# Performance work log

Measured on AMD Instinct MI355X. Metric: run time of the kernel, lower is better.

Reference implementation:

```python
import jax, jax.numpy as jnp
from jax import lax
import numpy as np

B, S, I, H, O, L = 64, 512, 1024, 1024, 1024, 2


def setup_inputs() -> dict:
    key = jax.random.key(0)
    ks = jax.random.split(key, 12)
    sI = 1.0 / np.sqrt(I)
    sH = 1.0 / np.sqrt(H)
    # weights stored as [in, out] (transpose of torch Linear.weight); same math.
    return {
        "input": jax.random.normal(ks[0], (B, S, I), jnp.float32),
        "Wxz": jax.random.uniform(ks[1], (L, I, H), jnp.float32, -sI, sI),
        "Whz": jax.random.uniform(ks[2], (L, H, H), jnp.float32, -sH, sH),
        "bz": jax.random.uniform(ks[3], (L, H), jnp.float32, -sH, sH),
        "Wxr": jax.random.uniform(ks[4], (L, I, H), jnp.float32, -sI, sI),
        "Whr": jax.random.uniform(ks[5], (L, H, H), jnp.float32, -sH, sH),
        "br": jax.random.uniform(ks[6], (L, H), jnp.float32, -sH, sH),
        "Wxg": jax.random.uniform(ks[7], (L, I, H), jnp.float32, -sI, sI),
        "Whg": jax.random.uniform(ks[8], (L, H, H), jnp.float32, -sH, sH),
        "bg": jax.random.uniform(ks[9], (L, H), jnp.float32, -sH, sH),
        "Why": jax.random.uniform(ks[10], (H, O), jnp.float32, -sH, sH),
        "by": jax.random.uniform(ks[11], (O,), jnp.float32, -sH, sH),
    }


def reference(input, Wxz, Whz, bz, Wxr, Whr, br, Wxg, Whg, bg, Why, by):
    n_layers = Whz.shape[0]
    batch = input.shape[0]
    h_dim = Whz.shape[-1]
    h0 = jnp.zeros((n_layers, batch, h_dim), input.dtype)  # (L,B,H)

    def step(h, xt):  # xt: (B,I)
        new_h = []
        inp = xt
        for l in range(n_layers):  # static, small
            hl = h[l]
            z = jax.nn.sigmoid(inp @ Wxz[l] + hl @ Whz[l] + bz[l])
            r = jax.nn.sigmoid(inp @ Wxr[l] + hl @ Whr[l] + br[l])
            g = jnp.tanh(inp @ Wxg[l] + (r * hl) @ Whg[l] + bg[l])
            hl = z * hl + (1.0 - z) * g
            new_h.append(hl)
            inp = hl
        y = inp @ Why + by  # (B,O)
        return jnp.stack(new_h), y

    hT, ys = lax.scan(step, h0, jnp.swapaxes(input, 0, 1))  # ys: (S,B,O)
    layer_output = jnp.swapaxes(ys, 0, 1)       # (B,S,O)
    hidden_state = jnp.swapaxes(hT, 0, 1)       # (B,L,H)
    return layer_output, hidden_state
```

## Files before the change

### kernel.cpp

```cpp
#include <hip/hip_runtime.h>
#include <cstdint>

using u16 = unsigned short;
using u32 = unsigned int;
using u64 = unsigned long long;

typedef __bf16 bf16x8 __attribute__((ext_vector_type(8)));
typedef float  f32x4  __attribute__((ext_vector_type(4)));
typedef unsigned int u32x4 __attribute__((ext_vector_type(4)));

#define WPITCH 2064
#define SCAN_LDS 124160
#define YG_LDS   147456
#define POLL_BOUND 32768

__device__ __forceinline__ float b2f(u16 u) {
    u32 i = ((u32)u) << 16; float f; __builtin_memcpy(&f, &i, 4); return f;
}
__device__ __forceinline__ u16 f2b(float f) {
    u32 i; __builtin_memcpy(&i, &f, 4);
    u32 r = (i + 0x7FFFu + ((i >> 16) & 1u)) >> 16; return (u16)r;
}
__device__ __forceinline__ uint4 pack8f(const float* f) {
    u16 t[8];
#pragma unroll
    for (int j = 0; j < 8; ++j) t[j] = f2b(f[j]);
    uint4 r; __builtin_memcpy(&r, t, 16); return r;
}

__global__ __launch_bounds__(512) void gru_fused(
    const float* __restrict__ xin,
    const float* __restrict__ Wxz, const float* __restrict__ Wxr,
    const float* __restrict__ Wxg,
    const float* __restrict__ Whz, const float* __restrict__ Whr,
    const float* __restrict__ Whg,
    const float* __restrict__ bzp, const float* __restrict__ brp,
    const float* __restrict__ bgp,
    float* __restrict__ hout,
    float* __restrict__ hidden,
    u16* __restrict__ ring,
    u16* __restrict__ hb,
    u16* __restrict__ rb,
    u32* __restrict__ flags)
{
    extern __shared__ char sm[];
    char*  hs    = sm;
    char*  scZ   = sm + 33024;
    char*  xb0   = sm + 65792;
    char*  xb1   = sm + 82176;
    float* xls   = (float*)(sm + 98560);
    u16*   tmp16 = (u16*)(sm + 123136);

    const int tid   = threadIdx.x;
    const int lane  = tid & 63;
    const int wv    = tid >> 6;
    const int layer = blockIdx.x >> 7;
    const int id    = blockIdx.x & 127;
    const int grp   = id >> 5;
    const int w     = id & 31;
    const int bg0   = grp * 16;
    const int n0w   = w * 32;
    const long wbase = (long)layer * 1048576;
    const long bbase = (long)layer * 1024;

    u16* hbG = hb + (layer * 4 + grp) * 16384;
    u16* rbG = rb + (layer * 4 + grp) * 16384;
    u32* f_rh   = flags + ((layer * 4 + grp) * 2 + 0) * 512;
    u32* f_h    = flags + ((layer * 4 + grp) * 2 + 1) * 512;
    u32* f_h_l0 = flags + ((0 * 4 + grp) * 2 + 1) * 512;
    u32* f_h_l1 = flags + ((1 * 4 + grp) * 2 + 1) * 512;

    bf16x8 wZ[2][4], wR[2][4], wG[2][4];
#pragma unroll
    for (int nt = 0; nt < 2; ++nt) {
#pragma unroll
        for (int i = 0; i < 4; ++i) {
            const int k0  = wv * 128 + i * 32 + ((lane >> 4) << 3);
            const int col = n0w + nt * 16 + (lane & 15);
            u16 ez[8], er[8], eg[8];
#pragma unroll
            for (int j = 0; j < 8; ++j) {
                long o = wbase + (long)(k0 + j) * 1024 + col;
                ez[j] = f2b(Whz[o]); er[j] = f2b(Whr[o]); eg[j] = f2b(Whg[o]);
            }
            __builtin_memcpy(&wZ[nt][i], ez, 16);
            __builtin_memcpy(&wR[nt][i], er, 16);
            __builtin_memcpy(&wG[nt][i], eg, 16);
        }
    }

    const int b8  = tid >> 5;
    const int n32 = tid & 31;
    const int ntc = n32 >> 4, nnc = n32 & 15;
    const int ls  = ((b8 >> 2) << 4) | nnc;
    const int el  = b8 & 3;
    const float biasZ = bzp[bbase + n0w + n32];
    const float biasR = brp[bbase + n0w + n32];
    const float biasG = bgp[bbase + n0w + n32];

    f32x4 aX0 = {0,0,0,0}, aX1 = {0,0,0,0};
    const int mT0 = (wv < 6) ? 0 : 1, nT0 = (wv < 6) ? wv : wv - 6;
    const int mT1 = 1, nT1 = 2 + wv;

    auto XLOAD = [&](int kt, int wt0, f32x4& ra, u64& rav, f32x4* rw) {
        int r = tid >> 4, j = tid & 15;
        if (layer == 0) {
            ra = *(const f32x4*)(xin +
                 ((long)(bg0 + (r & 15)) * 512 + (wt0 + (r >> 4))) * 1024 +
                 kt * 64 + j * 4);
        } else {
            const char* p = (const char*)ring +
                ((long)(((wt0 + (r >> 4)) & 7) * 64 + bg0 + (r & 15)) * 1024 +
                 kt * 64 + j * 4) * 2;
            asm volatile("global_load_dwordx2 %0, %1, off sc0 sc1\n\t"
                         "s_waitcnt vmcnt(0)"
                         : "=v"(rav) : "v"(p) : "memory");
        }
        if (tid >= 128) {
            int u = tid - 128, g3 = u >> 7, rem = u & 127, k = rem >> 1,
                half = rem & 1;
            const float* Wp = (g3 == 0 ? Wxz : (g3 == 1 ? Wxr : Wxg)) + wbase +
                              (long)(kt * 64 + k) * 1024 + n0w + half * 16;
            rw[0] = *(const f32x4*)(Wp);
            rw[1] = *(const f32x4*)(Wp + 4);
            rw[2] = *(const f32x4*)(Wp + 8);
            rw[3] = *(const f32x4*)(Wp + 12);
        }
    };
    auto XSTORE = [&](char* xb, const f32x4& ra, u64 rav, const f32x4* rw) {
        char* sA = xb; char* sW = xb + 4096;
        int r = tid >> 4, j = tid & 15;
        u64 v;
        if (layer == 0) {
            u16 e[4];
#pragma unroll
            for (int q = 0; q < 4; ++q) e[q] = f2b(ra[q]);
            __builtin_memcpy(&v, e, 8);
        } else v = rav;
        *(u64*)(sA + r * 128 + ((j * 8) ^ ((r & 7) << 4))) = v;
        if (tid >= 128) {
            int u = tid - 128, g3 = u >> 7, rem = u & 127, k = rem >> 1,
                half = rem & 1;
#pragma unroll
            for (int c = 0; c < 16; ++c) {
                int row = g3 * 32 + half * 16 + c;
                *(u16*)(sW + row * 128 + ((k * 2) ^ ((row & 7) << 4))) =
                    f2b(rw[c >> 2][c & 3]);
            }
        }
    };
    auto XMFMA = [&](char* xb) {
        char* sA = xb; char* sW = xb + 4096;
#pragma unroll
        for (int ks = 0; ks < 2; ++ks) {
            int kb = ks * 64 + ((lane >> 4) << 4);
            {
                int ar = mT0 * 16 + (lane & 15), br_ = nT0 * 16 + (lane & 15);
                bf16x8 aF = *(const bf16x8*)(sA + ar * 128 + (kb ^ ((ar & 7) << 4)));
                bf16x8 bF = *(const bf16x8*)(sW + br_ * 128 + (kb ^ ((br_ & 7) << 4)));
                aX0 = __builtin_amdgcn_mfma_f32_16x16x32_bf16(aF, bF, aX0, 0, 0, 0);
            }
            if (wv < 4) {
                int ar = mT1 * 16 + (lane & 15), br_ = nT1 * 16 + (lane & 15);
                bf16x8 aF = *(const bf16x8*)(sA + ar * 128 + (kb ^ ((ar & 7) << 4)));
                bf16x8 bF = *(const bf16x8*)(sW + br_ * 128 + (kb ^ ((br_ & 7) << 4)));
                aX1 = __builtin_amdgcn_mfma_f32_16x16x32_bf16(aF, bF, aX1, 0, 0, 0);
            }
        }
    };
    auto XP4 = [&](int kt0, int wt0, f32x4& ra, u64& rav, f32x4* rw) {
        XSTORE(xb0, ra, rav, rw);
        __syncthreads();
        XMFMA(xb0);
        XLOAD(kt0 + 1, wt0, ra, rav, rw);
        XSTORE(xb1, ra, rav, rw);
        __syncthreads();
        XMFMA(xb1);
        XLOAD(kt0 + 2, wt0, ra, rav, rw);
        XSTORE(xb0, ra, rav, rw);
        __syncthreads();
        XMFMA(xb0);
        XLOAD(kt0 + 3, wt0, ra, rav, rw);
        XSTORE(xb1, ra, rav, rw);
        __syncthreads();
        XMFMA(xb1);
    };
    auto XWRITE = [&](int buf) {
#pragma unroll
        for (int q = 0; q < 4; ++q) {
            int row = mT0 * 16 + ((lane >> 4) << 2) + q;
            xls[((buf * 2 + mT0) * 16 + (row & 15)) * 96 + nT0 * 16 + (lane & 15)] = aX0[q];
            if (wv < 4) {
                int row1 = 16 + ((lane >> 4) << 2) + q;
                xls[((buf * 2 + 1) * 16 + (row1 & 15)) * 96 + nT1 * 16 + (lane & 15)] = aX1[q];
            }
        }
        aX0 = (f32x4){0,0,0,0}; aX1 = (f32x4){0,0,0,0};
    };
    auto STAGE32 = [&](const char* src) {
        u32x4 a0, a1, a2, a3;
        const char* p = src + tid * 16;
        asm volatile(
            "global_load_dwordx4 %0, %4, off sc0 sc1\n\t"
            "global_load_dwordx4 %1, %5, off sc0 sc1\n\t"
            "global_load_dwordx4 %2, %6, off sc0 sc1\n\t"
            "global_load_dwordx4 %3, %7, off sc0 sc1\n\t"
            "s_waitcnt vmcnt(0)"
            : "=&v"(a0), "=&v"(a1), "=&v"(a2), "=&v"(a3)
            : "v"(p), "v"(p + 8192), "v"(p + 16384), "v"(p + 24576)
            : "memory");
        u32x4 a[4] = {a0, a1, a2, a3};
#pragma unroll
        for (int u = 0; u < 4; ++u) {
            int idx = u * 512 + tid;
            *(u32x4*)(hs + (idx >> 7) * WPITCH +
                      (((idx & 127) * 16) ^ (((idx >> 7) & 7) << 4))) = a[u];
        }
    };
    auto PUBLISH = [&](char* dst) {
        if (tid < 64) {
            int b = tid >> 2, q = tid & 3;
            u16 e[8];
#pragma unroll
            for (int j = 0; j < 8; ++j) e[j] = tmp16[b * 32 + q * 8 + j];
            u32x4 v; __builtin_memcpy(&v, e, 16);
            char* p = dst + b * 2048 + n0w * 2 + q * 16;
            asm volatile("global_store_dwordx4 %0, %1, off sc0 sc1"
                         :: "v"(p), "v"(v) : "memory");
        }
    };
    auto FLAGREL = [&](u32* fp, u32 tgtv) {
        if (tid == 0)
            asm volatile("s_waitcnt vmcnt(0)\n\t"
                         "global_store_dword %0, %1, off sc0 sc1"
                         :: "v"(fp), "v"(tgtv) : "memory");
    };
    auto FLAGWAIT = [&](const u32* fpbase, u32 tgtv) {
        if (tid < 32) {
            const u32* fp = fpbase + tid * 16;
            u32 v; int itc = 0;
            for (;;) {
                asm volatile("global_load_dword %0, %1, off sc0 sc1\n\t"
                             "s_waitcnt vmcnt(0)"
                             : "=v"(v) : "v"(fp) : "memory");
                if (v >= tgtv) break;
                if (++itc > POLL_BOUND) break;
                __builtin_amdgcn_s_sleep(1);
            }
        }
        __builtin_amdgcn_sched_barrier(0);
        __syncthreads();
    };

    {
        if (layer == 1) FLAGWAIT(f_h_l0, 2);
        f32x4 ra; u64 rav = 0; f32x4 rw[4];
        for (int kt = 0; kt < 16; kt += 4) {
            XLOAD(kt, 0, ra, rav, rw);
            XP4(kt, 0, ra, rav, rw);
        }
        __syncthreads();
        XWRITE(0);
        __syncthreads();
    }

    float h_own = 0.f;
    for (int tc = 0; tc < 512; ++tc) {
        const bool prod = (tc < 510);
        const int wt0 = (tc & ~1) + 2;
        const int kb8 = (tc & 1) * 8;
        const int buf = (tc >> 1) & 1;
        const int tl  = tc & 1;

        if (layer == 1 && (tc & 1) == 0 && prod)
            FLAGWAIT(f_h_l0, tc + 4);
        if (layer == 0 && tc >= 8)
            FLAGWAIT(f_h_l1, (u32)(tc - 8));

        f32x4 ra; u64 rav = 0; f32x4 rw[4];
        if (prod) {
            XLOAD(kb8 + 0, wt0, ra, rav, rw);
            XP4(kb8 + 0, wt0, ra, rav, rw);
        }

        if (tc == 0) {
            __syncthreads();
#pragma unroll
            for (int u = 0; u < 4; ++u) {
                int idx = u * 512 + tid;
                *(u32x4*)(hs + (idx >> 7) * WPITCH +
                          (((idx & 127) * 16) ^ (((idx >> 7) & 7) << 4))) =
                    (u32x4){0, 0, 0, 0};
            }
        } else {
            FLAGWAIT(f_h, (u32)tc);
            if (layer == 0)
                STAGE32((const char*)ring + (((tc - 1) & 7) * 64 + bg0) * 2048);
            else
                STAGE32((const char*)hbG);
        }
        __syncthreads();

        {
            f32x4 aZ0 = {0,0,0,0}, aZ1 = {0,0,0,0};
            f32x4 aR0 = {0,0,0,0}, aR1 = {0,0,0,0};
#pragma unroll
            for (int i = 0; i < 4; ++i) {
                int kby = wv * 256 + i * 64 + ((lane >> 4) << 4);
                int ar = lane & 15;
                bf16x8 aF = *(const bf16x8*)(hs + ar * WPITCH + (kby ^ ((ar & 7) << 4)));
                aZ0 = __builtin_amdgcn_mfma_f32_16x16x32_bf16(aF, wZ[0][i], aZ0, 0, 0, 0);
                aZ1 = __builtin_amdgcn_mfma_f32_16x16x32_bf16(aF, wZ[1][i], aZ1, 0, 0, 0);
                aR0 = __builtin_amdgcn_mfma_f32_16x16x32_bf16(aF, wR[0][i], aR0, 0, 0, 0);
                aR1 = __builtin_amdgcn_mfma_f32_16x16x32_bf16(aF, wR[1][i], aR1, 0, 0, 0);
            }
            *(f32x4*)(scZ + ((0 * 8 + wv) * 64 + lane) * 16) = aZ0;
            *(f32x4*)(scZ + ((1 * 8 + wv) * 64 + lane) * 16) = aZ1;
            *(f32x4*)(scZ + ((2 * 8 + wv) * 64 + lane) * 16) = aR0;
            *(f32x4*)(scZ + ((3 * 8 + wv) * 64 + lane) * 16) = aR1;
        }
        __syncthreads();

        float zval;
        {
            float sz = 0.f, sr = 0.f;
#pragma unroll
            for (int ww = 0; ww < 8; ++ww) {
                sz += *(const float*)(scZ + (((ntc)     * 8 + ww) * 64 + ls) * 16 + el * 4);
                sr += *(const float*)(scZ + (((2 + ntc) * 8 + ww) * 64 + ls) * 16 + el * 4);
            }
            const float* xrow = xls + ((buf * 2 + tl) * 16 + b8) * 96;
            sz += xrow[n32] + biasZ;
            sr += xrow[32 + n32] + biasR;
            zval = 1.f / (1.f + __expf(-sz));
            float rv = 1.f / (1.f + __expf(-sr));
            tmp16[b8 * 32 + n32] = f2b(rv * h_own);
        }
        __syncthreads();

        PUBLISH((char*)rbG);
        FLAGREL(f_rh + w * 16, (u32)(tc + 1));

        if (prod) {
            XLOAD(kb8 + 4, wt0, ra, rav, rw);
            XP4(kb8 + 4, wt0, ra, rav, rw);
        }

        FLAGWAIT(f_rh, (u32)(tc + 1));
        STAGE32((const char*)rbG);
        __syncthreads();

        {
            f32x4 aG0 = {0,0,0,0}, aG1 = {0,0,0,0};
#pragma unroll
            for (int i = 0; i < 4; ++i) {
                int kby = wv * 256 + i * 64 + ((lane >> 4) << 4);
                int ar = lane & 15;
                bf16x8 aF = *(const bf16x8*)(hs + ar * WPITCH + (kby ^ ((ar & 7) << 4)));
                aG0 = __builtin_amdgcn_mfma_f32_16x16x32_bf16(aF, wG[0][i], aG0, 0, 0, 0);
                aG1 = __builtin_amdgcn_mfma_f32_16x16x32_bf16(aF, wG[1][i], aG1, 0, 0, 0);
            }
            *(f32x4*)(scZ + ((0 * 8 + wv) * 64 + lane) * 16) = aG0;
            *(f32x4*)(scZ + ((1 * 8 + wv) * 64 + lane) * 16) = aG1;
        }
        __syncthreads();

        {
            float sg = 0.f;
#pragma unroll
            for (int ww = 0; ww < 8; ++ww)
                sg += *(const float*)(scZ + ((ntc * 8 + ww) * 64 + ls) * 16 + el * 4);
            sg += xls[((buf * 2 + tl) * 16 + b8) * 96 + 64 + n32] + biasG;
            float e  = __expf(-2.f * sg);
            float gt = 2.f / (1.f + e) - 1.f;
            float hn = zval * h_own + (1.f - zval) * gt;
            h_own = hn;
            tmp16[b8 * 32 + n32] = f2b(hn);
            if (layer == 1)
                hout[((long)(bg0 + b8) * 512 + tc) * 1024 + n0w + n32] = hn;
            if (tc == 511)
                hidden[(long)(bg0 + b8) * 2048 + layer * 1024 + n0w + n32] = hn;
        }
        __syncthreads();

        PUBLISH(layer == 0
                    ? (char*)ring + (((tc & 7) * 64 + bg0) * 2048)
                    : (char*)hbG);
        FLAGREL(f_h + w * 16, (u32)(tc + 1));

        if (tl == 1 && prod) {
            __syncthreads();
            XWRITE(buf ^ 1);
        }
    }
}

__global__ __launch_bounds__(256) void ygemm(const float* __restrict__ Why,
                                             const float* __restrict__ by,
                                             float* __restrict__ y)
{
    extern __shared__ char sm[];
    char* sA = sm;
    char* sW = sm + 131072;

    const int tid  = threadIdx.x;
    const int lane = tid & 63;
    const int wv   = tid >> 6;
    const long r0  = (long)blockIdx.x * 64;

    for (int it = 0; it < 32; ++it) {
        int c = it * 256 + tid;
        int row = c >> 7, j = c & 127;
        long gi = (r0 + row) * 1024 + j * 8;
        float tp[8];
        *(uint4*)tp       = *(const uint4*)(y + gi);
        *(uint4*)(tp + 4) = *(const uint4*)(y + gi + 4);
        *(uint4*)(sA + row * 2048 + ((j * 16) ^ ((row & 7) << 4))) = pack8f(tp);
    }
    __syncthreads();

    for (int nt = 0; nt < 8; ++nt) {
        f32x4 acc[4][2] = {};
        for (int kt = 0; kt < 16; ++kt) {
            __syncthreads();
#pragma unroll
            for (int uu = 0; uu < 4; ++uu) {
                int u = uu * 256 + tid;
                int nrow = u >> 3, jc = u & 7;
                u16 e[8];
#pragma unroll
                for (int q = 0; q < 8; ++q)
                    e[q] = f2b(Why[(long)(kt * 64 + jc * 8 + q) * 1024 + nt * 128 + nrow]);
                uint4 v; __builtin_memcpy(&v, e, 16);
                *(uint4*)(sW + nrow * 128 + ((jc * 16) ^ ((nrow & 7) << 4))) = v;
            }
            __syncthreads();
#pragma unroll
            for (int ks = 0; ks < 2; ++ks) {
                int kbA = kt * 128 + ks * 64 + ((lane >> 4) << 4);
                int kbW = ks * 64 + ((lane >> 4) << 4);
#pragma unroll
                for (int cc = 0; cc < 2; ++cc) {
                    int brr = (wv * 2 + cc) * 16 + (lane & 15);
                    bf16x8 bF = *(const bf16x8*)(sW + brr * 128 + (kbW ^ ((brr & 7) << 4)));
#pragma unroll
                    for (int m = 0; m < 4; ++m) {
                        int ar = m * 16 + (lane & 15);
                        bf16x8 aF = *(const bf16x8*)(sA + ar * 2048 + (kbA ^ ((ar & 7) << 4)));
                        acc[m][cc] = __builtin_amdgcn_mfma_f32_16x16x32_bf16(
                            aF, bF, acc[m][cc], 0, 0, 0);
                    }
                }
            }
        }
#pragma unroll
        for (int cc = 0; cc < 2; ++cc) {
            int col = nt * 128 + (wv * 2 + cc) * 16 + (lane & 15);
            float bv = by[col];
#pragma unroll
            for (int m = 0; m < 4; ++m)
#pragma unroll
                for (int q = 0; q < 4; ++q) {
                    long row = r0 + m * 16 + ((lane >> 4) << 2) + q;
                    y[row * 1024 + col] = acc[m][cc][q] + bv;
                }
        }
    }
}

extern "C" void kernel_launch(void* const* d_in, const int* in_sizes, int n_in,
                              void* d_out, int out_size, void* d_ws,
                              size_t ws_size, hipStream_t stream) {
    const float* input = (const float*)d_in[0];
    const float* Wxz = (const float*)d_in[1];
    const float* Whz = (const float*)d_in[2];
    const float* bz  = (const float*)d_in[3];
    const float* Wxr = (const float*)d_in[4];
    const float* Whr = (const float*)d_in[5];
    const float* br  = (const float*)d_in[6];
    const float* Wxg = (const float*)d_in[7];
    const float* Whg = (const float*)d_in[8];
    const float* bg  = (const float*)d_in[9];
    const float* Why = (const float*)d_in[10];
    const float* by  = (const float*)d_in[11];
    (void)in_sizes; (void)n_in; (void)out_size; (void)ws_size;

    float* yreg   = (float*)d_out;
    float* hidden = yreg + 33554432;

    char* ws = (char*)d_ws;
    u32* flags = (u32*)ws;
    u16* hb    = (u16*)(ws + 32768);
    u16* rb    = (u16*)(ws + 294912);
    u16* ring  = (u16*)(ws + 557056);

    hipFuncSetAttribute(reinterpret_cast<const void*>(gru_fused),
                        hipFuncAttributeMaxDynamicSharedMemorySize, SCAN_LDS);
    hipFuncSetAttribute(reinterpret_cast<const void*>(ygemm),
                        hipFuncAttributeMaxDynamicSharedMemorySize, YG_LDS);
    hipMemsetAsync(flags, 0, 32768, stream);

    gru_fused<<<256, 512, SCAN_LDS, stream>>>(
        input, Wxz, Wxr, Wxg, Whz, Whr, Whg, bz, br, bg,
        yreg, hidden, ring, hb, rb, flags);
    ygemm<<<512, 256, YG_LDS, stream>>>(Why, by, yreg);
}
```

Measured before the change: 12.07 ms.

## Quad-buffer input-projection tiles and prefetch across phases with register staging

Adds two more LDS staging buffers and restructures the input-projection K loop so two k-tiles are stored per barrier. Global loads for the next tiles are issued before MFMAs and carried across phase and timestep boundaries in register structs, which halves the barriers. Loads are widened to 16-byte per thread with a different thread mapping, and the layer-1 flag wait moves earlier to cover the prefetch. This costs more LDS and registers, which may reduce occupancy, and the cross-step dependency ordering becomes more complex.

```diff
diff --git a/kernel.cpp b/kernel.cpp
--- a/kernel.cpp
+++ b/kernel.cpp
@@ -10,7 +10,7 @@
 typedef unsigned int u32x4 __attribute__((ext_vector_type(4)));
 
 #define WPITCH 2064
-#define SCAN_LDS 124160
+#define SCAN_LDS 156928
 #define YG_LDS   147456
 #define POLL_BOUND 32768
 
@@ -27,6 +27,8 @@
     for (int j = 0; j < 8; ++j) t[j] = f2b(f[j]);
     uint4 r; __builtin_memcpy(&r, t, 16); return r;
 }
+
+struct XReg { f32x4 a0, a1; u64 v0, v1; f32x4 w0, w1, w2, w3; };
 
 __global__ __launch_bounds__(512) void gru_fused(
     const float* __restrict__ xin,
@@ -48,8 +50,10 @@
     char*  scZ   = sm + 33024;
     char*  xb0   = sm + 65792;
     char*  xb1   = sm + 82176;
-    float* xls   = (float*)(sm + 98560);
-    u16*   tmp16 = (u16*)(sm + 123136);
+    char*  xb2   = sm + 98560;
+    char*  xb3   = sm + 114944;
+    float* xls   = (float*)(sm + 131328);
+    u16*   tmp16 = (u16*)(sm + 155904);
 
     const int tid   = threadIdx.x;
     const int lane  = tid & 63;
@@ -102,50 +106,61 @@
     const int mT0 = (wv < 6) ? 0 : 1, nT0 = (wv < 6) ? wv : wv - 6;
     const int mT1 = 1, nT1 = 2 + wv;
 
-    auto XLOAD = [&](int kt, int wt0, f32x4& ra, u64& rav, f32x4* rw) {
-        int r = tid >> 4, j = tid & 15;
-        if (layer == 0) {
-            ra = *(const f32x4*)(xin +
-                 ((long)(bg0 + (r & 15)) * 512 + (wt0 + (r >> 4))) * 1024 +
-                 kt * 64 + j * 4);
-        } else {
-            const char* p = (const char*)ring +
-                ((long)(((wt0 + (r >> 4)) & 7) * 64 + bg0 + (r & 15)) * 1024 +
-                 kt * 64 + j * 4) * 2;
-            asm volatile("global_load_dwordx2 %0, %1, off sc0 sc1\n\t"
-                         "s_waitcnt vmcnt(0)"
-                         : "=v"(rav) : "v"(p) : "memory");
-        }
-        if (tid >= 128) {
-            int u = tid - 128, g3 = u >> 7, rem = u & 127, k = rem >> 1,
+    auto XISSUE = [&](int kt, int wt0, XReg& X) {
+        if (tid >= 256) {
+            int u = tid - 256, r = u >> 3, j = u & 7;
+            if (layer == 0) {
+                const float* p = xin +
+                    ((long)(bg0 + (r & 15)) * 512 + (wt0 + (r >> 4))) * 1024 +
+                    kt * 64 + j * 8;
+                X.a0 = *(const f32x4*)p;
+                X.a1 = *(const f32x4*)(p + 4);
+            } else {
+                const u64* p = (const u64*)((const char*)ring +
+                    ((long)(((wt0 + (r >> 4)) & 7) * 64 + bg0 + (r & 15)) * 1024 +
+                     kt * 64 + j * 8) * 2);
+                X.v0 = __hip_atomic_load(p, __ATOMIC_RELAXED,
+                                         __HIP_MEMORY_SCOPE_AGENT);
+                X.v1 = __hip_atomic_load(p + 1, __ATOMIC_RELAXED,
+                                         __HIP_MEMORY_SCOPE_AGENT);
+            }
+        }
+        if (tid >= 64 && tid < 448) {
+            int u = tid - 64, g3 = u >> 7, rem = u & 127, k = rem >> 1,
                 half = rem & 1;
             const float* Wp = (g3 == 0 ? Wxz : (g3 == 1 ? Wxr : Wxg)) + wbase +
                               (long)(kt * 64 + k) * 1024 + n0w + half * 16;
-            rw[0] = *(const f32x4*)(Wp);
-            rw[1] = *(const f32x4*)(Wp + 4);
-            rw[2] = *(const f32x4*)(Wp + 8);
-            rw[3] = *(const f32x4*)(Wp + 12);
-        }
-    };
-    auto XSTORE = [&](char* xb, const f32x4& ra, u64 rav, const f32x4* rw) {
+            X.w0 = *(const f32x4*)(Wp);
+            X.w1 = *(const f32x4*)(Wp + 4);
+            X.w2 = *(const f32x4*)(Wp + 8);
+            X.w3 = *(const f32x4*)(Wp + 12);
+        }
+    };
+    auto XSTORE = [&](char* xb, const XReg& X) {
         char* sA = xb; char* sW = xb + 4096;
-        int r = tid >> 4, j = tid & 15;
-        u64 v;
-        if (layer == 0) {
-            u16 e[4];
-#pragma unroll
-            for (int q = 0; q < 4; ++q) e[q] = f2b(ra[q]);
-            __builtin_memcpy(&v, e, 8);
-        } else v = rav;
-        *(u64*)(sA + r * 128 + ((j * 8) ^ ((r & 7) << 4))) = v;
-        if (tid >= 128) {
-            int u = tid - 128, g3 = u >> 7, rem = u & 127, k = rem >> 1,
+        if (tid >= 256) {
+            int u = tid - 256, r = u >> 3, j = u & 7;
+            uint4 val;
+            if (layer == 0) {
+                float t[8];
+                *(f32x4*)t       = X.a0;
+                *(f32x4*)(t + 4) = X.a1;
+                val = pack8f(t);
+            } else {
+                __builtin_memcpy(&val, &X.v0, 8);
+                __builtin_memcpy(((char*)&val) + 8, &X.v1, 8);
+            }
+            *(uint4*)(sA + r * 128 + ((j * 16) ^ ((r & 7) << 4))) = val;
+        }
+        if (tid >= 64 && tid < 448) {
+            int u = tid - 64, g3 = u >> 7, rem = u & 127, k = rem >> 1,
                 half = rem & 1;
+            f32x4 wv4[4] = {X.w0, X.w1, X.w2, X.w3};
 #pragma unroll
             for (int c = 0; c < 16; ++c) {
                 int row = g3 * 32 + half * 16 + c;
                 *(u16*)(sW + row * 128 + ((k * 2) ^ ((row & 7) << 4))) =
-                    f2b(rw[c >> 2][c & 3]);
+                    f2b(wv4[c >> 2][c & 3]);
             }
         }
     };
@@ -168,22 +183,21 @@
             }
         }
     };
-    auto XP4 = [&](int kt0, int wt0, f32x4& ra, u64& rav, f32x4* rw) {
-        XSTORE(xb0, ra, rav, rw);
+    auto XP4 = [&](int kt0, int wt0, XReg& A, XReg& B, int nkt, int nwt0,
+                   bool dn) {
+        XSTORE(xb0, A);
+        XSTORE(xb1, B);
+        XISSUE(kt0 + 2, wt0, A);
+        XISSUE(kt0 + 3, wt0, B);
         __syncthreads();
         XMFMA(xb0);
-        XLOAD(kt0 + 1, wt0, ra, rav, rw);
-        XSTORE(xb1, ra, rav, rw);
-        __syncthreads();
         XMFMA(xb1);
-        XLOAD(kt0 + 2, wt0, ra, rav, rw);
-        XSTORE(xb0, ra, rav, rw);
-        __syncthreads();
-        XMFMA(xb0);
-        XLOAD(kt0 + 3, wt0, ra, rav, rw);
-        XSTORE(xb1, ra, rav, rw);
-        __syncthreads();
-        XMFMA(xb1);
+        XSTORE(xb2, A);
+        XSTORE(xb3, B);
+        if (dn) { XISSUE(nkt, nwt0, A); XISSUE(nkt + 1, nwt0, B); }
+        __syncthreads();
+        XMFMA(xb2);
+        XMFMA(xb3);
     };
     auto XWRITE = [&](int buf) {
 #pragma unroll
@@ -252,13 +266,15 @@
         __syncthreads();
     };
 
+    XReg A, B;
     {
-        if (layer == 1) FLAGWAIT(f_h_l0, 2);
-        f32x4 ra; u64 rav = 0; f32x4 rw[4];
-        for (int kt = 0; kt < 16; kt += 4) {
-            XLOAD(kt, 0, ra, rav, rw);
-            XP4(kt, 0, ra, rav, rw);
-        }
+        if (layer == 1) FLAGWAIT(f_h_l0, 4);
+        XISSUE(0, 0, A);
+        XISSUE(1, 0, B);
+        XP4(0, 0, A, B, 4, 0, true);
+        XP4(4, 0, A, B, 8, 0, true);
+        XP4(8, 0, A, B, 12, 0, true);
+        XP4(12, 0, A, B, 0, 2, true);
         __syncthreads();
         XWRITE(0);
         __syncthreads();
@@ -272,16 +288,10 @@
         const int buf = (tc >> 1) & 1;
         const int tl  = tc & 1;
 
-        if (layer == 1 && (tc & 1) == 0 && prod)
-            FLAGWAIT(f_h_l0, tc + 4);
         if (layer == 0 && tc >= 8)
             FLAGWAIT(f_h_l1, (u32)(tc - 8));
 
-        f32x4 ra; u64 rav = 0; f32x4 rw[4];
-        if (prod) {
-            XLOAD(kb8 + 0, wt0, ra, rav, rw);
-            XP4(kb8 + 0, wt0, ra, rav, rw);
-        }
+        if (prod) XP4(kb8 + 0, wt0, A, B, -1, -1, false);
 
         if (tc == 0) {
             __syncthreads();
@@ -342,8 +352,14 @@
         FLAGREL(f_rh + w * 16, (u32)(tc + 1));
 
         if (prod) {
-            XLOAD(kb8 + 4, wt0, ra, rav, rw);
-            XP4(kb8 + 4, wt0, ra, rav, rw);
+            const bool dn  = (tc + 1 < 510);
+            if (layer == 1 && tl == 1 && dn)
+                FLAGWAIT(f_h_l0, (u32)(tc + 5));
+            XISSUE(kb8 + 4, wt0, A);
+            XISSUE(kb8 + 5, wt0, B);
+            const int nkb  = ((tc + 1) & 1) * 8;
+            const int nwt  = ((tc + 1) & ~1) + 2;
+            XP4(kb8 + 4, wt0, A, B, nkb, nwt, dn);
         }
 
         FLAGWAIT(f_rh, (u32)(tc + 1));
```

Result: no change. 11.98 ms (-0.7%).
